# Performance work log

Hardware: AMD Instinct MI355X
Metric: run time of the kernel (lower is better)

## Reference

```python
import jax, jax.numpy as jnp
import numpy as np

D_STATE = 4
DT_RANK = 4  # ceil(64/16)
D_INNER = 64


def conv1d(x, w, b, pad):
    # x: [B,C,L], w: [O,I,K]
    y = jax.lax.conv_general_dilated(x, w, (1,), [(pad, pad)],
                                     dimension_numbers=('NCH', 'OIH', 'NCH'))
    return y + b[None, :, None]


def maxpool2(x):
    B, C, L = x.shape
    return x.reshape(B, C, L // 2, 2).max(-1)


def layernorm(x, g, b):
    m = x.mean(-1, keepdims=True)
    v = ((x - m) ** 2).mean(-1, keepdims=True)
    return (x - m) / jnp.sqrt(v + 1e-5) * g + b


def mamba_block(x, in_w, cv_w, cv_b, xp_w, dt_w, dt_b, A_log, Dp, out_w):
    # x: [B,L,d_model]; d_inner == d_model (expand=1)
    B, L, _ = x.shape
    xz = jnp.einsum('bld,ed->ble', x, in_w)          # [B,L,2*d_inner]
    xi, z = jnp.split(xz, 2, axis=-1)
    # causal depthwise conv, kernel size 2
    xc = jax.lax.conv_general_dilated(xi.transpose(0, 2, 1), cv_w, (1,), [(1, 0)],
                                      feature_group_count=D_INNER,
                                      dimension_numbers=('NCH', 'OIH', 'NCH'))
    u = jax.nn.silu(xc + cv_b[None, :, None]).transpose(0, 2, 1)  # [B,L,d_inner]
    x_dbl = jnp.einsum('bld,ed->ble', u, xp_w)        # [B,L,dt_rank+2*d_state]
    dt, Bm, Cm = jnp.split(x_dbl, [DT_RANK, DT_RANK + D_STATE], axis=-1)
    dt = jax.nn.softplus(jnp.einsum('blr,dr->bld', dt, dt_w) + dt_b)  # [B,L,d_inner]
    A = -jnp.exp(A_log)                               # [d_inner, d_state]
    dA = jnp.exp(dt[..., None] * A)                   # [B,L,d_inner,d_state]
    dBu = dt[..., None] * Bm[:, :, None, :] * u[..., None]

    def step(h, inp):
        dA_t, dBu_t, C_t = inp
        h = dA_t * h + dBu_t                          # [B,d_inner,d_state]
        y = jnp.einsum('bdn,bn->bd', h, C_t)
        return h, y

    h0 = jnp.zeros((B, D_INNER, D_STATE), x.dtype)
    _, ys = jax.lax.scan(step, h0, (dA.transpose(1, 0, 2, 3),
                                    dBu.transpose(1, 0, 2, 3),
                                    Cm.transpose(1, 0, 2)))
    y = ys.transpose(1, 0, 2) + Dp * u                # skip connection D*u
    y = y * jax.nn.silu(z)
    return jnp.einsum('bld,ed->ble', y, out_w)


def setup_inputs() -> dict:
    key = jax.random.key(0)
    ks = jax.random.split(key, 32)
    n = lambda k, s, sc=0.05: (jax.random.normal(k, s, jnp.float32) * sc)
    inp = {
        'x': jax.random.normal(ks[0], (512, 1, 4096), jnp.float32),
        'c1w': n(ks[1], (16, 1, 5), 0.3), 'c1b': n(ks[2], (16,)),
        'c2w': n(ks[3], (32, 16, 5), 0.1), 'c2b': n(ks[4], (32,)),
        'c3w': n(ks[5], (64, 32, 5), 0.08), 'c3b': n(ks[6], (64,)),
        'lw': n(ks[7], (4096, 2048), 0.02), 'lb': n(ks[8], (4096,)),
    }
    A_init = jnp.log(jnp.tile(jnp.arange(1, D_STATE + 1, dtype=jnp.float32), (D_INNER, 1)))
    for i, base in ((1, 9), (2, 20)):
        inp[f'ln{i}g'] = jnp.ones((64,), jnp.float32)
        inp[f'ln{i}b'] = jnp.zeros((64,), jnp.float32)
        inp[f'in{i}w'] = n(ks[base + 0], (2 * D_INNER, 64), 0.08)
        inp[f'cv{i}w'] = n(ks[base + 1], (D_INNER, 1, 2), 0.3)
        inp[f'cv{i}b'] = n(ks[base + 2], (D_INNER,))
        inp[f'xp{i}w'] = n(ks[base + 3], (DT_RANK + 2 * D_STATE, D_INNER), 0.08)
        inp[f'dt{i}w'] = n(ks[base + 4], (D_INNER, DT_RANK), 0.3)
        inp[f'dt{i}b'] = n(ks[base + 5], (D_INNER,), 0.5)
        inp[f'al{i}'] = A_init
        inp[f'dp{i}'] = jnp.ones((D_INNER,), jnp.float32)
        inp[f'ow{i}'] = n(ks[base + 6], (64, D_INNER), 0.08)
    return inp


def reference(x, c1w, c1b, c2w, c2b, c3w, c3b, lw, lb,
              ln1g, ln1b, in1w, cv1w, cv1b, xp1w, dt1w, dt1b, al1, dp1, ow1,
              ln2g, ln2b, in2w, cv2w, cv2b, xp2w, dt2w, dt2b, al2, dp2, ow2):
    B = x.shape[0]
    h = maxpool2(jax.nn.relu(conv1d(x, c1w, c1b, 2)))       # [B,16,L/2]
    h = maxpool2(jax.nn.relu(conv1d(h, c2w, c2b, 2)))       # [B,32,L/4]
    h = jax.nn.relu(conv1d(h, c3w, c3b, 2))                 # [B,64,L/4]
    # AdaptiveAvgPool1d(32): L/4 divisible by 32 -> exact window means
    L4 = h.shape[-1]
    h = h.reshape(B, 64, 32, L4 // 32).mean(-1)             # [B,64,32]
    h = h.reshape(B, -1)                                    # [B,2048]
    h = (h @ lw.T + lb).reshape(B, 64, 64)                  # [B,64,64]
    h = mamba_block(layernorm(h, ln1g, ln1b), in1w, cv1w, cv1b, xp1w, dt1w, dt1b, al1, dp1, ow1)
    h = mamba_block(layernorm(h, ln2g, ln2b), in2w, cv2w, cv2b, xp2w, dt2w, dt2b, al2, dp2, ow2)
    return h
```

## Files before the change

kernel.cpp:

```cpp
#include <hip/hip_runtime.h>
#include <hip/hip_bf16.h>
#include <math.h>

#define NB 512

typedef __attribute__((ext_vector_type(8))) short short8;
typedef __attribute__((ext_vector_type(4))) float f32x4;
union U4 { uint4 u; short8 s8; };
union BF { __hip_bfloat16 h; ushort us; };

__device__ __forceinline__ int swz(int u) { return u ^ ((u >> 3) & 7); }
__device__ __forceinline__ int idx8(int l, int u) { return l * 8 + (u ^ (l & 7)); }

__global__ __launch_bounds__(256) void prep_w(const float* __restrict__ w2,
                                              __hip_bfloat16* __restrict__ w2b,
                                              const float* __restrict__ w3,
                                              __hip_bfloat16* __restrict__ w3b,
                                              const float* __restrict__ in1w,
                                              const float* __restrict__ in2w,
                                              __hip_bfloat16* __restrict__ winb,
                                              const float* __restrict__ ow1,
                                              const float* __restrict__ ow2,
                                              __hip_bfloat16* __restrict__ owb) {
    int i = blockIdx.x * 256 + threadIdx.x;
    if (i < 3072) {
        int c2 = i / 96, rest = i - c2 * 96;
        int tp = rest >> 5, r2 = rest & 31;
        int tl = r2 >> 4, c1 = r2 & 15;
        int tap = tp * 2 + tl;
        float v = (tap < 5) ? w2[c2 * 80 + c1 * 5 + tap] : 0.f;
        w2b[i] = __float2bfloat16(v);
    } else if (i < 13312) {
        int j = i - 3072;
        int c3 = j / 160, rest = j - c3 * 160;
        int kk = rest >> 5, c1 = rest & 31;
        w3b[j] = __float2bfloat16(w3[c3 * 160 + c1 * 5 + kk]);
    } else if (i < 29696) {
        int j = i - 13312;
        winb[j] = __float2bfloat16((j < 8192 ? in1w : in2w)[j & 8191]);
    } else {
        int j = i - 29696;
        owb[j] = __float2bfloat16((j < 4096 ? ow1 : ow2)[j & 4095]);
    }
}

__global__ __launch_bounds__(256) void conv_trunk(const float* __restrict__ x,
                                                  const float* __restrict__ c1w,
                                                  const float* __restrict__ c1b,
                                                  const __hip_bfloat16* __restrict__ w2b,
                                                  const float* __restrict__ c2b,
                                                  const __hip_bfloat16* __restrict__ w3b,
                                                  const float* __restrict__ c3b,
                                                  __hip_bfloat16* __restrict__ h3b) {
    __shared__ uint4 H1u[1088];
    __shared__ uint4 H2u[1088];
    float* xs = (float*)H2u;
    int t = threadIdx.x, h = blockIdx.x, b = blockIdx.y;
    int lane = t & 63, w = t >> 6, m = lane & 15, quad = lane >> 4;
    int p0 = h * 512 - 6;
    int gbase = h * 1024 - 14;

    const float* xb = x + b * 4096;
    for (int i = t; i < 1080; i += 256) {
        int gx = gbase + i;
        xs[i] = (gx >= 0 && gx < 4096) ? xb[gx] : 0.f;
    }
    U4 Bf2[3][2];
    {
        const uint4* wsrc = (const uint4*)w2b;
#pragma unroll
        for (int ct = 0; ct < 2; ++ct)
#pragma unroll
            for (int tp = 0; tp < 3; ++tp)
                Bf2[tp][ct].u = wsrc[(ct * 16 + m) * 12 + tp * 4 + quad];
    }
    float bv2[2];
#pragma unroll
    for (int ct = 0; ct < 2; ++ct) bv2[ct] = c2b[ct * 16 + m];
    float wv[80], bv1[16];
#pragma unroll
    for (int i = 0; i < 80; ++i) wv[i] = c1w[i];
#pragma unroll
    for (int i = 0; i < 16; ++i) bv1[i] = c1b[i];
    __syncthreads();

    for (int r = t; r < 536; r += 256) {
        int p = p0 + r;
        union { uint4 q[2]; __hip_bfloat16 hh[16]; } o;
        if (p >= 0 && p < 2048) {
            const float* s = xs + 2 * r;
            float s0 = s[0], s1 = s[1], s2 = s[2], s3 = s[3], s4 = s[4], s5 = s[5];
#pragma unroll
            for (int c = 0; c < 16; ++c) {
                const float* wr = wv + c * 5;
                float v0 = fmaf(wr[0], s0, fmaf(wr[1], s1, fmaf(wr[2], s2, fmaf(wr[3], s3, fmaf(wr[4], s4, bv1[c])))));
                float v1 = fmaf(wr[0], s1, fmaf(wr[1], s2, fmaf(wr[2], s3, fmaf(wr[3], s4, fmaf(wr[4], s5, bv1[c])))));
                o.hh[c] = __float2bfloat16(fmaxf(fmaxf(v0, v1), 0.f));
            }
        } else {
            o.q[0] = (uint4){0, 0, 0, 0};
            o.q[1] = (uint4){0, 0, 0, 0};
        }
        H1u[swz(2 * r)] = o.q[0];
        H1u[swz(2 * r + 1)] = o.q[1];
    }
    __syncthreads();

    __hip_bfloat16* H2h = (__hip_bfloat16*)H2u;
    for (int g = w; g < 33; g += 4) {
        f32x4 acc[2];
#pragma unroll
        for (int ct = 0; ct < 2; ++ct) acc[ct] = (f32x4){bv2[ct], bv2[ct], bv2[ct], bv2[ct]};
#pragma unroll
        for (int tp = 0; tp < 3; ++tp) {
            int u = 2 * (g * 16 + m + 2 * tp) + quad;
            U4 av; av.u = H1u[swz(u)];
            acc[0] = __builtin_amdgcn_mfma_f32_16x16x32_bf16(av.s8, Bf2[tp][0].s8, acc[0], 0, 0, 0);
            acc[1] = __builtin_amdgcn_mfma_f32_16x16x32_bf16(av.s8, Bf2[tp][1].s8, acc[1], 0, 0, 0);
        }
        int pp = g * 8 + quad * 2;
#pragma unroll
        for (int ct = 0; ct < 2; ++ct) {
            float o0 = fmaxf(fmaxf(acc[ct][0], acc[ct][1]), 0.f);
            float o1 = fmaxf(fmaxf(acc[ct][2], acc[ct][3]), 0.f);
            int ch = ct * 16 + m;
            int u0 = pp * 4 + (ch >> 3);
            H2h[swz(u0) * 8 + (ch & 7)] = __float2bfloat16(o0);
            H2h[swz(u0 + 4) * 8 + (ch & 7)] = __float2bfloat16(o1);
        }
    }
    __syncthreads();
    if (h == 0 && t < 8) H2u[swz((t >> 2) * 4 + (t & 3))] = (uint4){0, 0, 0, 0};
    if (h == 3 && t < 8) H2u[swz((258 + (t >> 2)) * 4 + (t & 3))] = (uint4){0, 0, 0, 0};
    __syncthreads();

    U4 Bf3[5][4];
    {
        const uint4* wsrc = (const uint4*)w3b;
#pragma unroll
        for (int ct = 0; ct < 4; ++ct)
#pragma unroll
            for (int kk = 0; kk < 5; ++kk)
                Bf3[kk][ct].u = wsrc[(ct * 16 + m) * 20 + kk * 4 + quad];
    }
    float bv3[4];
#pragma unroll
    for (int ct = 0; ct < 4; ++ct) bv3[ct] = c3b[ct * 16 + m];

#pragma unroll
    for (int ww = 0; ww < 2; ++ww) {
        int wl = w * 2 + ww;
        float sum[4] = {0.f, 0.f, 0.f, 0.f};
#pragma unroll
        for (int half = 0; half < 2; ++half) {
            int gp = wl * 2 + half;
            f32x4 acc[4];
#pragma unroll
            for (int ct = 0; ct < 4; ++ct) acc[ct] = (f32x4){bv3[ct], bv3[ct], bv3[ct], bv3[ct]};
#pragma unroll
            for (int kk = 0; kk < 5; ++kk) {
                int u = 4 * (gp * 16 + m + kk) + quad;
                U4 av; av.u = H2u[swz(u)];
#pragma unroll
                for (int ct = 0; ct < 4; ++ct)
                    acc[ct] = __builtin_amdgcn_mfma_f32_16x16x32_bf16(av.s8, Bf3[kk][ct].s8, acc[ct], 0, 0, 0);
            }
#pragma unroll
            for (int ct = 0; ct < 4; ++ct) {
                sum[ct] += fmaxf(acc[ct][0], 0.f) + fmaxf(acc[ct][1], 0.f)
                         + fmaxf(acc[ct][2], 0.f) + fmaxf(acc[ct][3], 0.f);
            }
        }
#pragma unroll
        for (int ct = 0; ct < 4; ++ct) {
            float s = sum[ct];
            s += __shfl_xor(s, 16, 64);
            s += __shfl_xor(s, 32, 64);
            sum[ct] = s;
        }
        float sv = (quad == 0) ? sum[0] : (quad == 1) ? sum[1] : (quad == 2) ? sum[2] : sum[3];
        int win = h * 8 + wl;
        h3b[b * 2048 + (quad * 16 + m) * 32 + win] = __float2bfloat16(sv * (1.f / 32.f));
    }
}

__global__ __launch_bounds__(256) void lin_gemm_mfma(const __hip_bfloat16* __restrict__ A,
                                                     const float* __restrict__ Bw,
                                                     const float* __restrict__ bias,
                                                     float* __restrict__ C) {
    __shared__ uint4 A_s[64 * 32];
    __shared__ uint4 B_s[64 * 32];
    int t = threadIdx.x;
    int col0 = blockIdx.x * 64;
    int row0 = blockIdx.y * 64;
    int w = t >> 6, lane = t & 63;
    int m = lane & 15, quad = lane >> 4;
    int lh = w >> 1, eh = w & 1;

    f32x4 acc[2][2];
#pragma unroll
    for (int li = 0; li < 2; ++li)
#pragma unroll
        for (int ei = 0; ei < 2; ++ei) acc[li][ei] = (f32x4){0.f, 0.f, 0.f, 0.f};

    uint4 pa[8];
    float4 pb[16];

#pragma unroll
    for (int p = 0; p < 8; ++p) {
        int id = p * 256 + t, r = id >> 5, u = id & 31;
        pa[p] = *(const uint4*)(A + (row0 + r) * 2048 + u * 8);
        const float4* s4 = (const float4*)(Bw + (size_t)(col0 + r) * 2048 + u * 8);
        pb[2 * p] = s4[0];
        pb[2 * p + 1] = s4[1];
    }

    for (int kt = 0; kt < 8; ++kt) {
#pragma unroll
        for (int p = 0; p < 8; ++p) {
            int id = p * 256 + t, r = id >> 5, u = id & 31;
            A_s[r * 32 + (u ^ (r & 31))] = pa[p];
            float4 f0 = pb[2 * p], f1 = pb[2 * p + 1];
            union { uint4 q; __hip_bfloat16 hh[8]; } o;
            o.hh[0] = __float2bfloat16(f0.x); o.hh[1] = __float2bfloat16(f0.y);
            o.hh[2] = __float2bfloat16(f0.z); o.hh[3] = __float2bfloat16(f0.w);
            o.hh[4] = __float2bfloat16(f1.x); o.hh[5] = __float2bfloat16(f1.y);
            o.hh[6] = __float2bfloat16(f1.z); o.hh[7] = __float2bfloat16(f1.w);
            B_s[r * 32 + (u ^ (r & 31))] = o.q;
        }
        __syncthreads();
        if (kt < 7) {
            int k0 = (kt + 1) * 256;
#pragma unroll
            for (int p = 0; p < 8; ++p) {
                int id = p * 256 + t, r = id >> 5, u = id & 31;
                pa[p] = *(const uint4*)(A + (row0 + r) * 2048 + k0 + u * 8);
                const float4* s4 = (const float4*)(Bw + (size_t)(col0 + r) * 2048 + k0 + u * 8);
                pb[2 * p] = s4[0];
                pb[2 * p + 1] = s4[1];
            }
        }
#pragma unroll
        for (int uu = 0; uu < 8; ++uu) {
            int ua = uu * 4 + quad;
            U4 av[2], bv[2];
#pragma unroll
            for (int li = 0; li < 2; ++li) {
                int ra = (lh * 2 + li) * 16 + m;
                av[li].u = A_s[ra * 32 + (ua ^ (ra & 31))];
            }
#pragma unroll
            for (int ei = 0; ei < 2; ++ei) {
                int rb = (eh * 2 + ei) * 16 + m;
                bv[ei].u = B_s[rb * 32 + (ua ^ (rb & 31))];
            }
#pragma unroll
            for (int li = 0; li < 2; ++li)
#pragma unroll
                for (int ei = 0; ei < 2; ++ei)
                    acc[li][ei] = __builtin_amdgcn_mfma_f32_16x16x32_bf16(av[li].s8, bv[ei].s8, acc[li][ei], 0, 0, 0);
        }
        __syncthreads();
    }
#pragma unroll
    for (int li = 0; li < 2; ++li)
#pragma unroll
        for (int ei = 0; ei < 2; ++ei) {
            int col = col0 + (eh * 2 + ei) * 16 + m;
            float bvv = bias[col];
#pragma unroll
            for (int reg = 0; reg < 4; ++reg) {
                int row = row0 + (lh * 2 + li) * 16 + quad * 4 + reg;
                C[row * 4096 + col] = acc[li][ei][reg] + bvv;
            }
        }
}

struct MambaP {
    const float *lng, *lnb, *cvw, *cvb, *xpw, *dtw, *dtb, *al, *dp;
};

__global__ __launch_bounds__(256) void mamba2_kernel(const float* __restrict__ lin,
                                                     const __hip_bfloat16* __restrict__ winb,
                                                     const __hip_bfloat16* __restrict__ owb,
                                                     MambaP p1, MambaP p2,
                                                     float* __restrict__ out) {
    __shared__ float X[64][68];
    __shared__ float XI[64][68];
    __shared__ float DTS[64][68];
    __shared__ float W12[64][14];
    __shared__ uint4 XBu[512];
    int b = blockIdx.x, t = threadIdx.x;
    int lane = t & 63, w = t >> 6, m = lane & 15, quad = lane >> 4;
    int l0 = w * 16;

    {
        const float4* lin4 = (const float4*)(lin + b * 4096);
        for (int i = t; i < 1024; i += 256) {
            float4 v = lin4[i];
            *(float4*)(&X[i >> 4][(i & 15) * 4]) = v;
        }
    }
    __syncthreads();

    for (int blk = 0; blk < 2; ++blk) {
        MambaP P = blk ? p2 : p1;

        {
            int l = t >> 2, q = t & 3;
            float4 xv[4];
            const float4* xr = (const float4*)(&X[l][q * 16]);
#pragma unroll
            for (int j = 0; j < 4; ++j) xv[j] = xr[j];
            float s = 0.f;
#pragma unroll
            for (int j = 0; j < 4; ++j) s += (xv[j].x + xv[j].y) + (xv[j].z + xv[j].w);
            s += __shfl_xor(s, 1, 4);
            s += __shfl_xor(s, 2, 4);
            float mm = s * (1.f / 64.f);
            float v = 0.f;
#pragma unroll
            for (int j = 0; j < 4; ++j) {
                float dx;
                dx = xv[j].x - mm; v = fmaf(dx, dx, v);
                dx = xv[j].y - mm; v = fmaf(dx, dx, v);
                dx = xv[j].z - mm; v = fmaf(dx, dx, v);
                dx = xv[j].w - mm; v = fmaf(dx, dx, v);
            }
            v += __shfl_xor(v, 1, 4);
            v += __shfl_xor(v, 2, 4);
            float rstd = rsqrtf(v * (1.f / 64.f) + 1e-5f);
            const float4* g4 = (const float4*)(P.lng + q * 16);
            const float4* bb4 = (const float4*)(P.lnb + q * 16);
            union { uint4 qq[2]; __hip_bfloat16 hh[16]; } o;
#pragma unroll
            for (int j = 0; j < 4; ++j) {
                float4 g = g4[j], bb = bb4[j];
                o.hh[j * 4 + 0] = __float2bfloat16((xv[j].x - mm) * rstd * g.x + bb.x);
                o.hh[j * 4 + 1] = __float2bfloat16((xv[j].y - mm) * rstd * g.y + bb.y);
                o.hh[j * 4 + 2] = __float2bfloat16((xv[j].z - mm) * rstd * g.z + bb.z);
                o.hh[j * 4 + 3] = __float2bfloat16((xv[j].w - mm) * rstd * g.w + bb.w);
            }
            XBu[idx8(l, q * 2)] = o.qq[0];
            XBu[idx8(l, q * 2 + 1)] = o.qq[1];
        }
        __syncthreads();

        {
            const uint4* wp = (const uint4*)winb + blk * 1024;
            U4 Bf[8][2];
#pragma unroll
            for (int nt = 0; nt < 8; ++nt)
#pragma unroll
                for (int c = 0; c < 2; ++c)
                    Bf[nt][c].u = wp[(nt * 16 + m) * 8 + c * 4 + quad];
            f32x4 acc[8];
#pragma unroll
            for (int nt = 0; nt < 8; ++nt) acc[nt] = (f32x4){0.f, 0.f, 0.f, 0.f};
#pragma unroll
            for (int c = 0; c < 2; ++c) {
                U4 av; av.u = XBu[idx8(l0 + m, c * 4 + quad)];
#pragma unroll
                for (int nt = 0; nt < 8; ++nt)
                    acc[nt] = __builtin_amdgcn_mfma_f32_16x16x32_bf16(av.s8, Bf[nt][c].s8, acc[nt], 0, 0, 0);
            }
#pragma unroll
            for (int nt = 0; nt < 4; ++nt)
#pragma unroll
                for (int reg = 0; reg < 4; ++reg)
                    XI[l0 + quad * 4 + reg][nt * 16 + m] = acc[nt][reg];
#pragma unroll
            for (int nt = 4; nt < 8; ++nt)
#pragma unroll
                for (int reg = 0; reg < 4; ++reg)
                    X[l0 + quad * 4 + reg][(nt - 4) * 16 + m] = acc[nt][reg];
        }
        __syncthreads();

        {
            int d = t & 63, lg = t >> 6;
            int lc = lg * 16;
            float cur[16];
            float prev = (lc == 0) ? 0.f : XI[lc - 1][d];
#pragma unroll
            for (int j = 0; j < 16; ++j) cur[j] = XI[lc + j][d];
            __syncthreads();
            float w0 = P.cvw[d * 2], w1 = P.cvw[d * 2 + 1], cb = P.cvb[d];
#pragma unroll
            for (int j = 0; j < 16; ++j) {
                float xp = (j == 0) ? prev : cur[j - 1];
                float v = fmaf(w0, xp, fmaf(w1, cur[j], cb));
                XI[lc + j][d] = v / (1.f + __expf(-v));
            }
        }
        __syncthreads();

        {
            int l = t & 63, jg = t >> 6;
            float4 xrow[16];
            const float4* xr = (const float4*)(&XI[l][0]);
#pragma unroll
            for (int k4 = 0; k4 < 16; ++k4) xrow[k4] = xr[k4];
#pragma unroll
            for (int jj = 0; jj < 3; ++jj) {
                int j = jg * 3 + jj;
                const float4* wr = (const float4*)(P.xpw + j * 64);
                float a0 = 0.f, a1 = 0.f, a2 = 0.f, a3 = 0.f;
#pragma unroll
                for (int k4 = 0; k4 < 16; ++k4) {
                    float4 wvv = wr[k4];
                    a0 = fmaf(xrow[k4].x, wvv.x, a0);
                    a1 = fmaf(xrow[k4].y, wvv.y, a1);
                    a2 = fmaf(xrow[k4].z, wvv.z, a2);
                    a3 = fmaf(xrow[k4].w, wvv.w, a3);
                }
                float accv = (a0 + a1) + (a2 + a3);
                int slot = (j < 4) ? j : ((j < 8) ? (4 + (j - 4) * 2) : (5 + (j - 8) * 2));
                W12[l][slot] = accv;
            }
        }
        __syncthreads();

        {
            int l = t & 63, dg = t >> 6;
            float d0 = W12[l][0], d1 = W12[l][1], d2 = W12[l][2], d3 = W12[l][3];
#pragma unroll 4
            for (int jj = 0; jj < 16; ++jj) {
                int d = dg * 16 + jj;
                const float4 wvv = *(const float4*)(P.dtw + d * 4);
                float xdt = fmaf(wvv.x, d0, fmaf(wvv.y, d1, fmaf(wvv.z, d2, fmaf(wvv.w, d3, P.dtb[d]))));
                DTS[d][l] = fmaxf(xdt, 0.f) + __logf(1.f + __expf(-fabsf(xdt)));
            }
        }
        __syncthreads();

        {
            int d = t >> 2, n = t & 3;
            float Aval = -__expf(P.al[d * 4 + n]);
            float dpv = P.dp[d];
            const float* dtrow = &DTS[d][0];
            ushort* YBh = (ushort*)XBu;
            float h = 0.f;
#pragma unroll 4
            for (int l = 0; l < 64; ++l) {
                float dtv = dtrow[l];
                float dA = __expf(dtv * Aval);
                float uv = XI[l][d];
                float2 bc = *(const float2*)(&W12[l][4 + n * 2]);
                h = fmaf(dA, h, dtv * bc.x * uv);
                float part = h * bc.y;
                part += __shfl_xor(part, 1, 4);
                part += __shfl_xor(part, 2, 4);
                if (n == 0) {
                    float zv = X[l][d];
                    float yv = part + dpv * uv;
                    float gy = yv * (zv / (1.f + __expf(-zv)));
                    BF cv; cv.h = __float2bfloat16(gy);
                    YBh[idx8(l, d >> 3) * 8 + (d & 7)] = cv.us;
                }
            }
        }
        __syncthreads();

        {
            const uint4* wp = (const uint4*)owb + blk * 512;
            U4 Bf[4][2];
#pragma unroll
            for (int nt = 0; nt < 4; ++nt)
#pragma unroll
                for (int c = 0; c < 2; ++c)
                    Bf[nt][c].u = wp[(nt * 16 + m) * 8 + c * 4 + quad];
            f32x4 acc[4];
#pragma unroll
            for (int nt = 0; nt < 4; ++nt) acc[nt] = (f32x4){0.f, 0.f, 0.f, 0.f};
#pragma unroll
            for (int c = 0; c < 2; ++c) {
                U4 av; av.u = XBu[idx8(l0 + m, c * 4 + quad)];
#pragma unroll
                for (int nt = 0; nt < 4; ++nt)
                    acc[nt] = __builtin_amdgcn_mfma_f32_16x16x32_bf16(av.s8, Bf[nt][c].s8, acc[nt], 0, 0, 0);
            }
            if (blk == 0) {
#pragma unroll
                for (int nt = 0; nt < 4; ++nt)
#pragma unroll
                    for (int reg = 0; reg < 4; ++reg)
                        X[l0 + quad * 4 + reg][nt * 16 + m] = acc[nt][reg];
            } else {
                float* ob = out + b * 4096;
#pragma unroll
                for (int nt = 0; nt < 4; ++nt)
#pragma unroll
                    for (int reg = 0; reg < 4; ++reg)
                        ob[(l0 + quad * 4 + reg) * 64 + nt * 16 + m] = acc[nt][reg];
            }
        }
        __syncthreads();
    }
}

extern "C" void kernel_launch(void* const* d_in, const int* in_sizes, int n_in,
                              void* d_out, int out_size, void* d_ws, size_t ws_size,
                              hipStream_t stream) {
    const float* x   = (const float*)d_in[0];
    const float* c1w = (const float*)d_in[1];
    const float* c1b = (const float*)d_in[2];
    const float* c2w = (const float*)d_in[3];
    const float* c2b = (const float*)d_in[4];
    const float* c3w = (const float*)d_in[5];
    const float* c3b = (const float*)d_in[6];
    const float* lw  = (const float*)d_in[7];
    const float* lb  = (const float*)d_in[8];

    MambaP p1, p2;
    p1.lng = (const float*)d_in[9];  p1.lnb = (const float*)d_in[10];
    p1.cvw = (const float*)d_in[12]; p1.cvb = (const float*)d_in[13];
    p1.xpw = (const float*)d_in[14]; p1.dtw = (const float*)d_in[15];
    p1.dtb = (const float*)d_in[16]; p1.al  = (const float*)d_in[17];
    p1.dp  = (const float*)d_in[18];
    p2.lng = (const float*)d_in[20]; p2.lnb = (const float*)d_in[21];
    p2.cvw = (const float*)d_in[23]; p2.cvb = (const float*)d_in[24];
    p2.xpw = (const float*)d_in[25]; p2.dtw = (const float*)d_in[26];
    p2.dtb = (const float*)d_in[27]; p2.al  = (const float*)d_in[28];
    p2.dp  = (const float*)d_in[29];
    const float* in1w = (const float*)d_in[11];
    const float* in2w = (const float*)d_in[22];
    const float* ow1  = (const float*)d_in[19];
    const float* ow2  = (const float*)d_in[30];

    const size_t MB = 1024 * 1024;
    char* base = (char*)d_ws;
    __hip_bfloat16* h3b  = (__hip_bfloat16*)base;
    float* lin           = (float*)(base + 4 * MB);
    __hip_bfloat16* w2b  = (__hip_bfloat16*)(base + 16 * MB);
    __hip_bfloat16* w3b  = (__hip_bfloat16*)(base + 16 * MB + 64 * 1024);
    __hip_bfloat16* winb = (__hip_bfloat16*)(base + 16 * MB + 256 * 1024);
    __hip_bfloat16* owb  = (__hip_bfloat16*)(base + 16 * MB + 512 * 1024);
    float* outp = (float*)d_out;

    prep_w<<<dim3(148), dim3(256), 0, stream>>>(c2w, w2b, c3w, w3b,
                                                in1w, in2w, winb, ow1, ow2, owb);
    conv_trunk<<<dim3(4, NB), dim3(256), 0, stream>>>(x, c1w, c1b, w2b, c2b, w3b, c3b, h3b);
    lin_gemm_mfma<<<dim3(64, 8), dim3(256), 0, stream>>>(h3b, lw, lb, lin);
    mamba2_kernel<<<dim3(NB), dim3(256), 0, stream>>>(lin, winb, owb, p1, p2, outp);
}
```

Baseline: 287.6 us.

## Fold weight prep into conv trunk and halve GEMM K-tile

Removes the separate weight-conversion kernel launch. Each conv_trunk block now builds its conv2/conv3 bf16 MFMA fragments directly from the fp32 weights with scalar gathers, and one block converts the mamba in/out projection weights. Separately, the linear GEMM moves from a 256-wide to a 128-wide K tile with half the prefetch registers and LDS, and adds a launch bound of 2 blocks per CU. The aim is to cut launch overhead and raise GEMM occupancy, at the cost of redundant uncoalesced weight loads in every conv block, one straggler block doing extra conversion work, and twice as many sync iterations in the GEMM.

```diff
diff --git a/kernel.cpp b/kernel.cpp
--- a/kernel.cpp
+++ b/kernel.cpp
@@ -12,45 +12,19 @@
 __device__ __forceinline__ int swz(int u) { return u ^ ((u >> 3) & 7); }
 __device__ __forceinline__ int idx8(int l, int u) { return l * 8 + (u ^ (l & 7)); }
 
-__global__ __launch_bounds__(256) void prep_w(const float* __restrict__ w2,
-                                              __hip_bfloat16* __restrict__ w2b,
-                                              const float* __restrict__ w3,
-                                              __hip_bfloat16* __restrict__ w3b,
-                                              const float* __restrict__ in1w,
-                                              const float* __restrict__ in2w,
-                                              __hip_bfloat16* __restrict__ winb,
-                                              const float* __restrict__ ow1,
-                                              const float* __restrict__ ow2,
-                                              __hip_bfloat16* __restrict__ owb) {
-    int i = blockIdx.x * 256 + threadIdx.x;
-    if (i < 3072) {
-        int c2 = i / 96, rest = i - c2 * 96;
-        int tp = rest >> 5, r2 = rest & 31;
-        int tl = r2 >> 4, c1 = r2 & 15;
-        int tap = tp * 2 + tl;
-        float v = (tap < 5) ? w2[c2 * 80 + c1 * 5 + tap] : 0.f;
-        w2b[i] = __float2bfloat16(v);
-    } else if (i < 13312) {
-        int j = i - 3072;
-        int c3 = j / 160, rest = j - c3 * 160;
-        int kk = rest >> 5, c1 = rest & 31;
-        w3b[j] = __float2bfloat16(w3[c3 * 160 + c1 * 5 + kk]);
-    } else if (i < 29696) {
-        int j = i - 13312;
-        winb[j] = __float2bfloat16((j < 8192 ? in1w : in2w)[j & 8191]);
-    } else {
-        int j = i - 29696;
-        owb[j] = __float2bfloat16((j < 4096 ? ow1 : ow2)[j & 4095]);
-    }
-}
-
 __global__ __launch_bounds__(256) void conv_trunk(const float* __restrict__ x,
                                                   const float* __restrict__ c1w,
                                                   const float* __restrict__ c1b,
-                                                  const __hip_bfloat16* __restrict__ w2b,
+                                                  const float* __restrict__ w2,
                                                   const float* __restrict__ c2b,
-                                                  const __hip_bfloat16* __restrict__ w3b,
+                                                  const float* __restrict__ w3,
                                                   const float* __restrict__ c3b,
+                                                  const float* __restrict__ in1w,
+                                                  const float* __restrict__ in2w,
+                                                  const float* __restrict__ ow1,
+                                                  const float* __restrict__ ow2,
+                                                  __hip_bfloat16* __restrict__ winb,
+                                                  __hip_bfloat16* __restrict__ owb,
                                                   __hip_bfloat16* __restrict__ h3b) {
     __shared__ uint4 H1u[1088];
     __shared__ uint4 H2u[1088];
@@ -65,15 +39,28 @@
         int gx = gbase + i;
         xs[i] = (gx >= 0 && gx < 4096) ? xb[gx] : 0.f;
     }
+    if (h == 1 && b == 0) {
+        for (int i = t; i < 16384; i += 256)
+            winb[i] = __float2bfloat16((i < 8192 ? in1w : in2w)[i & 8191]);
+        for (int i = t; i < 8192; i += 256)
+            owb[i] = __float2bfloat16((i < 4096 ? ow1 : ow2)[i & 4095]);
+    }
     U4 Bf2[3][2];
-    {
-        const uint4* wsrc = (const uint4*)w2b;
-#pragma unroll
-        for (int ct = 0; ct < 2; ++ct)
-#pragma unroll
-            for (int tp = 0; tp < 3; ++tp)
-                Bf2[tp][ct].u = wsrc[(ct * 16 + m) * 12 + tp * 4 + quad];
-    }
+#pragma unroll
+    for (int ct = 0; ct < 2; ++ct)
+#pragma unroll
+        for (int tp = 0; tp < 3; ++tp) {
+            union { uint4 q; __hip_bfloat16 hh[8]; } o;
+#pragma unroll
+            for (int j = 0; j < 8; ++j) {
+                int g = tp * 32 + quad * 8 + j;
+                int tl = (g >> 4) & 1, c1 = g & 15;
+                int tap = tp * 2 + tl;
+                float v = (tap < 5) ? w2[(ct * 16 + m) * 80 + c1 * 5 + tap] : 0.f;
+                o.hh[j] = __float2bfloat16(v);
+            }
+            Bf2[tp][ct].u = o.q;
+        }
     float bv2[2];
 #pragma unroll
     for (int ct = 0; ct < 2; ++ct) bv2[ct] = c2b[ct * 16 + m];
@@ -135,14 +122,18 @@
     __syncthreads();
 
     U4 Bf3[5][4];
-    {
-        const uint4* wsrc = (const uint4*)w3b;
-#pragma unroll
-        for (int ct = 0; ct < 4; ++ct)
-#pragma unroll
-            for (int kk = 0; kk < 5; ++kk)
-                Bf3[kk][ct].u = wsrc[(ct * 16 + m) * 20 + kk * 4 + quad];
-    }
+#pragma unroll
+    for (int ct = 0; ct < 4; ++ct)
+#pragma unroll
+        for (int kk = 0; kk < 5; ++kk) {
+            union { uint4 q; __hip_bfloat16 hh[8]; } o;
+#pragma unroll
+            for (int j = 0; j < 8; ++j) {
+                int c1 = quad * 8 + j;
+                o.hh[j] = __float2bfloat16(w3[(ct * 16 + m) * 160 + c1 * 5 + kk]);
+            }
+            Bf3[kk][ct].u = o.q;
+        }
     float bv3[4];
 #pragma unroll
     for (int ct = 0; ct < 4; ++ct) bv3[ct] = c3b[ct * 16 + m];
@@ -184,18 +175,19 @@
     }
 }
 
-__global__ __launch_bounds__(256) void lin_gemm_mfma(const __hip_bfloat16* __restrict__ A,
-                                                     const float* __restrict__ Bw,
-                                                     const float* __restrict__ bias,
-                                                     float* __restrict__ C) {
-    __shared__ uint4 A_s[64 * 32];
-    __shared__ uint4 B_s[64 * 32];
+__global__ __launch_bounds__(256, 2) void lin_gemm_mfma(const __hip_bfloat16* __restrict__ A,
+                                                        const float* __restrict__ Bw,
+                                                        const float* __restrict__ bias,
+                                                        float* __restrict__ C) {
+    __shared__ uint4 A_s[64 * 16];
+    __shared__ uint4 B_s[64 * 16];
     int t = threadIdx.x;
     int col0 = blockIdx.x * 64;
     int row0 = blockIdx.y * 64;
     int w = t >> 6, lane = t & 63;
     int m = lane & 15, quad = lane >> 4;
     int lh = w >> 1, eh = w & 1;
+    int pr = t >> 4, pu = t & 15;
 
     f32x4 acc[2][2];
 #pragma unroll
@@ -203,56 +195,56 @@
 #pragma unroll
         for (int ei = 0; ei < 2; ++ei) acc[li][ei] = (f32x4){0.f, 0.f, 0.f, 0.f};
 
-    uint4 pa[8];
-    float4 pb[16];
-
-#pragma unroll
-    for (int p = 0; p < 8; ++p) {
-        int id = p * 256 + t, r = id >> 5, u = id & 31;
-        pa[p] = *(const uint4*)(A + (row0 + r) * 2048 + u * 8);
-        const float4* s4 = (const float4*)(Bw + (size_t)(col0 + r) * 2048 + u * 8);
+    uint4 pa[4];
+    float4 pb[8];
+
+#pragma unroll
+    for (int p = 0; p < 4; ++p) {
+        int r = pr + p * 16;
+        pa[p] = *(const uint4*)(A + (row0 + r) * 2048 + pu * 8);
+        const float4* s4 = (const float4*)(Bw + (size_t)(col0 + r) * 2048 + pu * 8);
         pb[2 * p] = s4[0];
         pb[2 * p + 1] = s4[1];
     }
 
-    for (int kt = 0; kt < 8; ++kt) {
-#pragma unroll
-        for (int p = 0; p < 8; ++p) {
-            int id = p * 256 + t, r = id >> 5, u = id & 31;
-            A_s[r * 32 + (u ^ (r & 31))] = pa[p];
+    for (int kt = 0; kt < 16; ++kt) {
+#pragma unroll
+        for (int p = 0; p < 4; ++p) {
+            int r = pr + p * 16;
+            A_s[r * 16 + (pu ^ (r & 15))] = pa[p];
             float4 f0 = pb[2 * p], f1 = pb[2 * p + 1];
             union { uint4 q; __hip_bfloat16 hh[8]; } o;
             o.hh[0] = __float2bfloat16(f0.x); o.hh[1] = __float2bfloat16(f0.y);
             o.hh[2] = __float2bfloat16(f0.z); o.hh[3] = __float2bfloat16(f0.w);
             o.hh[4] = __float2bfloat16(f1.x); o.hh[5] = __float2bfloat16(f1.y);
             o.hh[6] = __float2bfloat16(f1.z); o.hh[7] = __float2bfloat16(f1.w);
-            B_s[r * 32 + (u ^ (r & 31))] = o.q;
-        }
-        __syncthreads();
-        if (kt < 7) {
-            int k0 = (kt + 1) * 256;
-#pragma unroll
-            for (int p = 0; p < 8; ++p) {
-                int id = p * 256 + t, r = id >> 5, u = id & 31;
-                pa[p] = *(const uint4*)(A + (row0 + r) * 2048 + k0 + u * 8);
-                const float4* s4 = (const float4*)(Bw + (size_t)(col0 + r) * 2048 + k0 + u * 8);
+            B_s[r * 16 + (pu ^ (r & 15))] = o.q;
+        }
+        __syncthreads();
+        if (kt < 15) {
+            int k0 = (kt + 1) * 128;
+#pragma unroll
+            for (int p = 0; p < 4; ++p) {
+                int r = pr + p * 16;
+                pa[p] = *(const uint4*)(A + (row0 + r) * 2048 + k0 + pu * 8);
+                const float4* s4 = (const float4*)(Bw + (size_t)(col0 + r) * 2048 + k0 + pu * 8);
                 pb[2 * p] = s4[0];
                 pb[2 * p + 1] = s4[1];
             }
         }
 #pragma unroll
-        for (int uu = 0; uu < 8; ++uu) {
-            int ua = uu * 4 + quad;
+        for (int c = 0; c < 4; ++c) {
+            int ua = c * 4 + quad;
             U4 av[2], bv[2];
 #pragma unroll
             for (int li = 0; li < 2; ++li) {
                 int ra = (lh * 2 + li) * 16 + m;
-                av[li].u = A_s[ra * 32 + (ua ^ (ra & 31))];
+                av[li].u = A_s[ra * 16 + (ua ^ (ra & 15))];
             }
 #pragma unroll
             for (int ei = 0; ei < 2; ++ei) {
                 int rb = (eh * 2 + ei) * 16 + m;
-                bv[ei].u = B_s[rb * 32 + (ua ^ (rb & 31))];
+                bv[ei].u = B_s[rb * 16 + (ua ^ (rb & 15))];
             }
 #pragma unroll
             for (int li = 0; li < 2; ++li)
@@ -532,15 +524,12 @@
     char* base = (char*)d_ws;
     __hip_bfloat16* h3b  = (__hip_bfloat16*)base;
     float* lin           = (float*)(base + 4 * MB);
-    __hip_bfloat16* w2b  = (__hip_bfloat16*)(base + 16 * MB);
-    __hip_bfloat16* w3b  = (__hip_bfloat16*)(base + 16 * MB + 64 * 1024);
-    __hip_bfloat16* winb = (__hip_bfloat16*)(base + 16 * MB + 256 * 1024);
-    __hip_bfloat16* owb  = (__hip_bfloat16*)(base + 16 * MB + 512 * 1024);
+    __hip_bfloat16* winb = (__hip_bfloat16*)(base + 16 * MB);
+    __hip_bfloat16* owb  = (__hip_bfloat16*)(base + 16 * MB + 256 * 1024);
     float* outp = (float*)d_out;
 
-    prep_w<<<dim3(148), dim3(256), 0, stream>>>(c2w, w2b, c3w, w3b,
-                                                in1w, in2w, winb, ow1, ow2, owb);
-    conv_trunk<<<dim3(4, NB), dim3(256), 0, stream>>>(x, c1w, c1b, w2b, c2b, w3b, c3b, h3b);
+    conv_trunk<<<dim3(4, NB), dim3(256), 0, stream>>>(x, c1w, c1b, c2w, c2b, c3w, c3b,
+                                                      in1w, in2w, ow1, ow2, winb, owb, h3b);
     lin_gemm_mfma<<<dim3(64, 8), dim3(256), 0, stream>>>(h3b, lw, lb, lin);
     mamba2_kernel<<<dim3(NB), dim3(256), 0, stream>>>(lin, winb, owb, p1, p2, outp);
 }
```

Result: slower. 347.7 us (+20.9%).
